# Kernel optimization log

Measured on AMD Instinct MI355X. Metric: run time of the kernel, lower is better.

## Reference

```python
import jax, jax.numpy as jnp
import numpy as np

TEMPERATURE = 0.1
NUM_CLASSES = 21
L2_EPS = 1e-12   # torch F.normalize eps
NEG = -1e9       # masking value for invalid (absent-class) logit slots


def setup_inputs() -> dict:
    key = jax.random.key(0)
    k1, k2 = jax.random.split(key)
    features = jax.random.normal(k1, (16, 512, 64, 64), dtype=jnp.float32)
    labels = jax.random.randint(k2, (16, 513, 513), 0, NUM_CLASSES, dtype=jnp.int32)
    return {"features": features, "labels": labels}


def reference(features, labels):
    B, D, H, W = features.shape
    C = NUM_CLASSES
    # torch: F.interpolate(labels.float()[:,None], (H,W), mode='bilinear').squeeze(1).long()
    lab = jax.image.resize(labels.astype(jnp.float32)[:, None], (B, 1, H, W),
                           method="bilinear", antialias=False)
    lab = lab[:, 0].astype(jnp.int32)                     # [B,H,W]

    # per-image, per-class masked feature pooling (segment reduce)
    masks = (lab[:, None, :, :] == jnp.arange(C)[None, :, None, None]).astype(features.dtype)  # [B,C,H,W]
    sums = jnp.einsum('bdhw,bchw->bcd', features, masks)  # [B,C,D]
    norms = jnp.linalg.norm(sums, axis=-1, keepdims=True)
    protos = sums / jnp.maximum(norms, L2_EPS)            # normalized prototypes [B,C,D]
    pres = masks.sum((2, 3)) > 0                          # [B,C] class present in image

    # all pairwise prototype dots: S[c,e,i,j] = <proto[i,c], proto[j,e]> / T
    S = jnp.einsum('icd,jed->ceij', protos, protos) / TEMPERATURE  # [C,C,B,B]
    presT = pres.T                                        # [C,B]
    valid = presT[:, None, :, None] & presT[None, :, None, :]       # [C,C,B,B]
    masked = jnp.where(valid, S, NEG)

    idx = jnp.arange(C)
    diag = masked[idx, idx]                               # [C,B,B] positive block S[c,c]
    dvalid = valid[idx, idx]                              # [C,B,B]

    # logits for class c = concat(p_block, all n_blocks) -> diag block appears twice
    lse_diag = jax.nn.logsumexp(diag, axis=(1, 2))        # [C]
    lse_all = jax.nn.logsumexp(masked, axis=(1, 2, 3))    # [C]
    lse = jnp.logaddexp(lse_diag, lse_all)                # [C]

    cnt = dvalid.sum((1, 2))
    pos_mean = jnp.where(dvalid, diag, 0.0).sum((1, 2)) / jnp.maximum(cnt, 1)

    cls_present = pres.any(0)                             # [C]
    loss = jnp.sum(jnp.where(cls_present, lse - pos_mean, 0.0))
    return loss
```

## Files before the change

kernel.cpp:

```cpp
#include <hip/hip_runtime.h>
#include <cstdint>
#include <cstddef>

#define NUM_C 21
#define NROW 336
#define N2   (NROW * NROW)
#define KSLABS 8

typedef __attribute__((ext_vector_type(8))) short short8;
typedef __attribute__((ext_vector_type(4))) float f32x4;
typedef __attribute__((ext_vector_type(4))) int int4v;

union frag_u { int4v i; short8 s; };
__device__ __forceinline__ short8 mk_frag(uint32_t a0, uint32_t a1, uint32_t a2, uint32_t a3) {
    frag_u u; u.i = int4v{(int)a0, (int)a1, (int)a2, (int)a3}; return u.s;
}
__device__ __forceinline__ uint32_t mask_pair(uint32_t eL, uint32_t eH, uint32_t c) {
    return (eL == c ? 0x3F80u : 0u) | (eH == c ? 0x3F800000u : 0u);
}

__global__ __launch_bounds__(256) void k1_resize_hist(const int* __restrict__ labels,
                                                      uint8_t* __restrict__ lab,
                                                      int* __restrict__ countsPart,
                                                      float* __restrict__ out) {
    int b = blockIdx.x >> 4, strip = blockIdx.x & 15;
    if (blockIdx.x == 0 && threadIdx.x == 0) out[0] = 0.0f;
    __shared__ int hist[NUM_C];
    if (threadIdx.x < NUM_C) hist[threadIdx.x] = 0;
    __syncthreads();

    int p = strip * 256 + threadIdx.x;
    int y = p >> 6, x = p & 63;
    const int* L = labels + (size_t)b * 263169;
    float sy = (y + 0.5f) * 8.015625f - 0.5f;
    float sx = (x + 0.5f) * 8.015625f - 0.5f;
    int y0 = (int)sy; float fy = sy - (float)y0;
    int x0 = (int)sx; float fx = sx - (float)x0;
    const int* r0 = L + y0 * 513 + x0;
    float L00 = (float)__builtin_nontemporal_load(r0);
    float L01 = (float)__builtin_nontemporal_load(r0 + 1);
    float L10 = (float)__builtin_nontemporal_load(r0 + 513);
    float L11 = (float)__builtin_nontemporal_load(r0 + 514);
    float v0 = (1.0f - fx) * L00 + fx * L01;
    float v1 = (1.0f - fx) * L10 + fx * L11;
    float val = (1.0f - fy) * v0 + fy * v1;
    int c = (int)val;
    lab[b * 4096 + p] = (uint8_t)c;
    atomicAdd(&hist[c], 1);
    __syncthreads();
    if (threadIdx.x < NUM_C) countsPart[blockIdx.x * NUM_C + threadIdx.x] = hist[threadIdx.x];
}

__global__ __launch_bounds__(256) void k2_sums(const float* __restrict__ feat,
                                               const uint8_t* __restrict__ lab,
                                               float* __restrict__ sums_part) {
    int bid = blockIdx.x;
    int b = bid >> 6, slab = (bid >> 3) & 7, ng = bid & 7;
    int t = threadIdx.x, wv = t >> 6, lane = t & 63;
    int nt = ng * 4 + wv;
    int d = nt * 16 + (lane & 15);
    int g8 = (lane >> 4) * 8;
    uint32_t c  = lane & 15;
    uint32_t c2 = c + 16;
    const float*   fp = feat + ((size_t)(b * 512 + d)) * 4096 + slab * 512 + g8;
    const uint8_t* lp = lab + b * 4096 + slab * 512 + g8;
    f32x4 acc0 = {0.f, 0.f, 0.f, 0.f}, acc1 = {0.f, 0.f, 0.f, 0.f};

#pragma unroll 2
    for (int ks = 0; ks < 16; ++ks) {
        f32x4 fA = __builtin_nontemporal_load((const f32x4*)fp);
        f32x4 fB = __builtin_nontemporal_load((const f32x4*)(fp + 4));
        uint32_t w0 = *(const uint32_t*)lp;
        uint32_t w1 = *(const uint32_t*)(lp + 4);
        fp += 32; lp += 32;

        uint32_t u0 = __float_as_uint(fA[0]), u1 = __float_as_uint(fA[1]),
                 u2 = __float_as_uint(fA[2]), u3 = __float_as_uint(fA[3]),
                 u4 = __float_as_uint(fB[0]), u5 = __float_as_uint(fB[1]),
                 u6 = __float_as_uint(fB[2]), u7 = __float_as_uint(fB[3]);
        short8 bHi = mk_frag(__builtin_amdgcn_perm(u1, u0, 0x07060302u),
                             __builtin_amdgcn_perm(u3, u2, 0x07060302u),
                             __builtin_amdgcn_perm(u5, u4, 0x07060302u),
                             __builtin_amdgcn_perm(u7, u6, 0x07060302u));
        float t0 = fA[0] - __uint_as_float(u0 & 0xFFFF0000u);
        float t1 = fA[1] - __uint_as_float(u1 & 0xFFFF0000u);
        float t2 = fA[2] - __uint_as_float(u2 & 0xFFFF0000u);
        float t3 = fA[3] - __uint_as_float(u3 & 0xFFFF0000u);
        float t4 = fB[0] - __uint_as_float(u4 & 0xFFFF0000u);
        float t5 = fB[1] - __uint_as_float(u5 & 0xFFFF0000u);
        float t6 = fB[2] - __uint_as_float(u6 & 0xFFFF0000u);
        float t7 = fB[3] - __uint_as_float(u7 & 0xFFFF0000u);
        short8 bLo = mk_frag(
            __builtin_amdgcn_perm(__float_as_uint(t1), __float_as_uint(t0), 0x07060302u),
            __builtin_amdgcn_perm(__float_as_uint(t3), __float_as_uint(t2), 0x07060302u),
            __builtin_amdgcn_perm(__float_as_uint(t5), __float_as_uint(t4), 0x07060302u),
            __builtin_amdgcn_perm(__float_as_uint(t7), __float_as_uint(t6), 0x07060302u));

        uint32_t e0 = w0 & 255u, e1 = (w0 >> 8) & 255u, e2 = (w0 >> 16) & 255u, e3 = w0 >> 24;
        uint32_t e4 = w1 & 255u, e5 = (w1 >> 8) & 255u, e6 = (w1 >> 16) & 255u, e7 = w1 >> 24;
        short8 a0 = mk_frag(mask_pair(e0, e1, c),  mask_pair(e2, e3, c),
                            mask_pair(e4, e5, c),  mask_pair(e6, e7, c));
        short8 a1 = mk_frag(mask_pair(e0, e1, c2), mask_pair(e2, e3, c2),
                            mask_pair(e4, e5, c2), mask_pair(e6, e7, c2));

        acc0 = __builtin_amdgcn_mfma_f32_16x16x32_bf16(a0, bHi, acc0, 0, 0, 0);
        acc1 = __builtin_amdgcn_mfma_f32_16x16x32_bf16(a1, bHi, acc1, 0, 0, 0);
        acc0 = __builtin_amdgcn_mfma_f32_16x16x32_bf16(a0, bLo, acc0, 0, 0, 0);
        acc1 = __builtin_amdgcn_mfma_f32_16x16x32_bf16(a1, bLo, acc1, 0, 0, 0);
    }

    int rowc = (lane >> 4) * 4;
    float* sp = sums_part + (size_t)slab * NROW * 512;
#pragma unroll
    for (int j = 0; j < 4; ++j) {
        sp[(size_t)((rowc + j) * 16 + b) * 512 + d] = acc0[j];
        if (rowc + j < 5)
            sp[(size_t)((16 + rowc + j) * 16 + b) * 512 + d] = acc1[j];
    }
}

__global__ __launch_bounds__(256) void k3_fold(const float4* __restrict__ part,
                                               float4* __restrict__ sums) {
    int idx = blockIdx.x * 256 + threadIdx.x;
    float4 s = part[idx];
#pragma unroll
    for (int q = 1; q < KSLABS; ++q) {
        float4 v = part[q * 43008 + idx];
        s.x += v.x; s.y += v.y; s.z += v.z; s.w += v.w;
    }
    sums[idx] = s;
}

__global__ __launch_bounds__(64) void k4_gram(const float* __restrict__ sums,
                                              float* __restrict__ gpart) {
    int row0 = blockIdx.x * 32, col0 = blockIdx.y * 32, k0 = blockIdx.z * 64;
    __shared__ float A[32 * 66], Bt[32 * 66];
    int t = threadIdx.x;
    int row = t >> 1, kk0 = (t & 1) * 32;
#pragma unroll
    for (int q = 0; q < 8; ++q) {
        int kk = kk0 + q * 4;
        int ra = row0 + row, rb = col0 + row;
        float4 va = (ra < NROW) ? *(const float4*)&sums[(size_t)ra * 512 + k0 + kk]
                                : make_float4(0.f, 0.f, 0.f, 0.f);
        float4 vb = (rb < NROW) ? *(const float4*)&sums[(size_t)rb * 512 + k0 + kk]
                                : make_float4(0.f, 0.f, 0.f, 0.f);
        *(float2*)&A[row * 66 + kk]      = make_float2(va.x, va.y);
        *(float2*)&A[row * 66 + kk + 2]  = make_float2(va.z, va.w);
        *(float2*)&Bt[row * 66 + kk]     = make_float2(vb.x, vb.y);
        *(float2*)&Bt[row * 66 + kk + 2] = make_float2(vb.z, vb.w);
    }
    __syncthreads();
    int ty = t >> 3, tx = t & 7;
    float acc[4][4] = {};
    for (int kk = 0; kk < 64; kk += 2) {
        float2 a[4], bb[4];
#pragma unroll
        for (int u = 0; u < 4; ++u) {
            a[u]  = *(const float2*)&A[(ty * 4 + u) * 66 + kk];
            bb[u] = *(const float2*)&Bt[(tx * 4 + u) * 66 + kk];
        }
#pragma unroll
        for (int u = 0; u < 4; ++u)
#pragma unroll
            for (int v = 0; v < 4; ++v)
                acc[u][v] += a[u].x * bb[v].x + a[u].y * bb[v].y;
    }
    float* gp = gpart + (size_t)blockIdx.z * N2;
#pragma unroll
    for (int u = 0; u < 4; ++u) {
        int r1 = row0 + ty * 4 + u;
        if (r1 >= NROW) continue;
        int r2 = col0 + tx * 4;
        if (r2 + 3 < NROW) {
            *(float4*)&gp[(size_t)r1 * NROW + r2] =
                make_float4(acc[u][0], acc[u][1], acc[u][2], acc[u][3]);
        } else {
#pragma unroll
            for (int v = 0; v < 4; ++v)
                if (r2 + v < NROW) gp[(size_t)r1 * NROW + r2 + v] = acc[u][v];
        }
    }
}

__global__ __launch_bounds__(1024) void k5_loss(const float* __restrict__ gpart,
                                                const int* __restrict__ countsPart,
                                                float* __restrict__ out) {
    int c = blockIdx.x, t = threadIdx.x;
    int wv = t >> 6, lane = t & 63;
    __shared__ float invnL[NROW];
    __shared__ uint8_t presL[NROW];
    __shared__ float redE[16], redD[16], redL[16];

    for (int r = t; r < NROW; r += 1024) {
        float ss = 0.0f;
#pragma unroll
        for (int s = 0; s < 8; ++s) ss += gpart[(size_t)s * N2 + (size_t)r * 337];
        invnL[r] = 1.0f / fmaxf(sqrtf(ss), 1e-12f);
        int img = r & 15, cls = r >> 4;
        int cnt = 0;
#pragma unroll
        for (int s = 0; s < 16; ++s) cnt += countsPart[(img * 16 + s) * NUM_C + cls];
        presL[r] = cnt > 0 ? 1 : 0;
    }
    __syncthreads();

    int nc = 0;
#pragma unroll
    for (int j = 0; j < 16; ++j) nc += presL[c * 16 + j];
    if (nc == 0) return;

    float eS = 0.0f, dE = 0.0f, dL = 0.0f;
    for (int idx = t; idx < 16 * NROW; idx += 1024) {
        int i = idx / NROW, r2 = idx - i * NROW;
        int r1 = c * 16 + i;
        float g = 0.0f;
#pragma unroll
        for (int s = 0; s < 8; ++s) g += gpart[(size_t)s * N2 + (size_t)r1 * NROW + r2];
        if (presL[r1] && presL[r2]) {
            float sv = g * invnL[r1] * invnL[r2] * 10.0f;
            float e = expf(sv - 10.0f);
            eS += e;
            if ((r2 >> 4) == c) { dE += e; dL += sv; }
        }
    }
#pragma unroll
    for (int off = 32; off >= 1; off >>= 1) {
        eS += __shfl_xor(eS, off, 64);
        dE += __shfl_xor(dE, off, 64);
        dL += __shfl_xor(dL, off, 64);
    }
    if (lane == 0) { redE[wv] = eS; redD[wv] = dE; redL[wv] = dL; }
    __syncthreads();
    if (t == 0) {
        float E = 0, D = 0, Ln = 0;
#pragma unroll
        for (int w = 0; w < 16; ++w) { E += redE[w]; D += redD[w]; Ln += redL[w]; }
        float lse = 10.0f + logf(E + D);
        float posMean = Ln / (float)(nc * nc);
        atomicAdd(out, lse - posMean);
    }
}

extern "C" void kernel_launch(void* const* d_in, const int* in_sizes, int n_in,
                              void* d_out, int out_size, void* d_ws, size_t ws_size,
                              hipStream_t stream) {
    const float* features = (const float*)d_in[0];
    const int* labels = (const int*)d_in[1];
    char* ws = (char*)d_ws;

    uint8_t* lab     = (uint8_t*)ws;
    int* countsPart  = (int*)(ws + 65536);
    float* sums_part = (float*)(ws + 87040);
    float* sums      = (float*)(ws + 87040 + 5505024);
    float* gpart     = (float*)(ws + 87040 + 5505024 + 688128);
    float* out       = (float*)d_out;

    k1_resize_hist<<<256, 256, 0, stream>>>(labels, lab, countsPart, out);
    k2_sums<<<1024, 256, 0, stream>>>(features, lab, sums_part);
    k3_fold<<<168, 256, 0, stream>>>((const float4*)sums_part, (float4*)sums);
    k4_gram<<<dim3(11, 11, 8), 64, 0, stream>>>(sums, gpart);
    k5_loss<<<21, 1024, 0, stream>>>(gpart, countsPart, out);
}
```

Measured before the change: 218.1 us.

## Switch class-pooling MFMA to 32x32x16 tiles with finer pixel slabs

The per-class feature pooling kernel now uses one 32x32x16 bf16 MFMA per hi/lo half instead of two 16x16x32 MFMAs over 16-class halves. One wave now covers 32 channels by 32 class slots, so the duplicated mask fragment and the padded 32-class work drop from four MFMAs per step to two. To keep the grid size, the pixel dimension is split into 16 slabs instead of 8. This doubles the partial-sum buffer and the work in the fold kernel. The accumulator grows to 16 floats per lane, and the launch bounds now request 4 blocks per CU.

```diff
diff --git a/kernel.cpp b/kernel.cpp
--- a/kernel.cpp
+++ b/kernel.cpp
@@ -5,10 +5,11 @@
 #define NUM_C 21
 #define NROW 336
 #define N2   (NROW * NROW)
-#define KSLABS 8
+#define KSLABS 16
 
 typedef __attribute__((ext_vector_type(8))) short short8;
 typedef __attribute__((ext_vector_type(4))) float f32x4;
+typedef __attribute__((ext_vector_type(16))) float f32x16;
 typedef __attribute__((ext_vector_type(4))) int int4v;
 
 union frag_u { int4v i; short8 s; };
@@ -51,28 +52,29 @@
     if (threadIdx.x < NUM_C) countsPart[blockIdx.x * NUM_C + threadIdx.x] = hist[threadIdx.x];
 }
 
-__global__ __launch_bounds__(256) void k2_sums(const float* __restrict__ feat,
-                                               const uint8_t* __restrict__ lab,
-                                               float* __restrict__ sums_part) {
+__global__ __launch_bounds__(256, 4) void k2_sums(const float* __restrict__ feat,
+                                                  const uint8_t* __restrict__ lab,
+                                                  float* __restrict__ sums_part) {
     int bid = blockIdx.x;
-    int b = bid >> 6, slab = (bid >> 3) & 7, ng = bid & 7;
+    int b = bid >> 6, slab = (bid >> 2) & 15, ng = bid & 3;
     int t = threadIdx.x, wv = t >> 6, lane = t & 63;
-    int nt = ng * 4 + wv;
-    int d = nt * 16 + (lane & 15);
-    int g8 = (lane >> 4) * 8;
-    uint32_t c  = lane & 15;
-    uint32_t c2 = c + 16;
-    const float*   fp = feat + ((size_t)(b * 512 + d)) * 4096 + slab * 512 + g8;
-    const uint8_t* lp = lab + b * 4096 + slab * 512 + g8;
-    f32x4 acc0 = {0.f, 0.f, 0.f, 0.f}, acc1 = {0.f, 0.f, 0.f, 0.f};
-
-#pragma unroll 2
-    for (int ks = 0; ks < 16; ++ks) {
-        f32x4 fA = __builtin_nontemporal_load((const f32x4*)fp);
-        f32x4 fB = __builtin_nontemporal_load((const f32x4*)(fp + 4));
-        uint32_t w0 = *(const uint32_t*)lp;
-        uint32_t w1 = *(const uint32_t*)(lp + 4);
-        fp += 32; lp += 32;
+    int g = lane >> 5;
+    int dbase = (ng * 4 + wv) * 32;
+    int d = dbase + (lane & 31);
+    uint32_t c = lane & 31;
+    const float*   fp = feat + ((size_t)(b * 512 + d)) * 4096 + slab * 256 + g * 128;
+    const uint8_t* lp = lab + b * 4096 + slab * 256 + g * 128;
+
+    f32x16 acc;
+#pragma unroll
+    for (int j = 0; j < 16; ++j) acc[j] = 0.0f;
+
+#pragma unroll 4
+    for (int s = 0; s < 16; ++s) {
+        f32x4 fA = __builtin_nontemporal_load((const f32x4*)(fp + s * 8));
+        f32x4 fB = __builtin_nontemporal_load((const f32x4*)(fp + s * 8 + 4));
+        uint32_t w0 = *(const uint32_t*)(lp + s * 8);
+        uint32_t w1 = *(const uint32_t*)(lp + s * 8 + 4);
 
         uint32_t u0 = __float_as_uint(fA[0]), u1 = __float_as_uint(fA[1]),
                  u2 = __float_as_uint(fA[2]), u3 = __float_as_uint(fA[3]),
@@ -98,24 +100,19 @@
 
         uint32_t e0 = w0 & 255u, e1 = (w0 >> 8) & 255u, e2 = (w0 >> 16) & 255u, e3 = w0 >> 24;
         uint32_t e4 = w1 & 255u, e5 = (w1 >> 8) & 255u, e6 = (w1 >> 16) & 255u, e7 = w1 >> 24;
-        short8 a0 = mk_frag(mask_pair(e0, e1, c),  mask_pair(e2, e3, c),
-                            mask_pair(e4, e5, c),  mask_pair(e6, e7, c));
-        short8 a1 = mk_frag(mask_pair(e0, e1, c2), mask_pair(e2, e3, c2),
-                            mask_pair(e4, e5, c2), mask_pair(e6, e7, c2));
-
-        acc0 = __builtin_amdgcn_mfma_f32_16x16x32_bf16(a0, bHi, acc0, 0, 0, 0);
-        acc1 = __builtin_amdgcn_mfma_f32_16x16x32_bf16(a1, bHi, acc1, 0, 0, 0);
-        acc0 = __builtin_amdgcn_mfma_f32_16x16x32_bf16(a0, bLo, acc0, 0, 0, 0);
-        acc1 = __builtin_amdgcn_mfma_f32_16x16x32_bf16(a1, bLo, acc1, 0, 0, 0);
-    }
-
-    int rowc = (lane >> 4) * 4;
+        short8 a = mk_frag(mask_pair(e0, e1, c), mask_pair(e2, e3, c),
+                           mask_pair(e4, e5, c), mask_pair(e6, e7, c));
+
+        acc = __builtin_amdgcn_mfma_f32_32x32x16_bf16(a, bHi, acc, 0, 0, 0);
+        acc = __builtin_amdgcn_mfma_f32_32x32x16_bf16(a, bLo, acc, 0, 0, 0);
+    }
+
     float* sp = sums_part + (size_t)slab * NROW * 512;
-#pragma unroll
-    for (int j = 0; j < 4; ++j) {
-        sp[(size_t)((rowc + j) * 16 + b) * 512 + d] = acc0[j];
-        if (rowc + j < 5)
-            sp[(size_t)((16 + rowc + j) * 16 + b) * 512 + d] = acc1[j];
+    int rb = 4 * g;
+#pragma unroll
+    for (int j = 0; j < 16; ++j) {
+        int row = (j & 3) + 8 * (j >> 2) + rb;
+        if (row < NUM_C) sp[(size_t)(row * 16 + b) * 512 + d] = acc[j];
     }
 }
 
@@ -252,8 +249,8 @@
     uint8_t* lab     = (uint8_t*)ws;
     int* countsPart  = (int*)(ws + 65536);
     float* sums_part = (float*)(ws + 87040);
-    float* sums      = (float*)(ws + 87040 + 5505024);
-    float* gpart     = (float*)(ws + 87040 + 5505024 + 688128);
+    float* sums      = (float*)(ws + 87040 + 11010048);
+    float* gpart     = (float*)(ws + 87040 + 11010048 + 688128);
     float* out       = (float*)d_out;
 
     k1_resize_hist<<<256, 256, 0, stream>>>(labels, lab, countsPart, out);
```

New measurement: 271.2 us. 24.3% more time.
